# Kernel optimization log

Measured on AMD Instinct MI355X. Metric: run time of the kernel, lower is better.

## Reference

```python
import jax, jax.numpy as jnp
import numpy as np

NEG_INF = -1.0e15  # matches the module's self.infty


def setup_inputs() -> dict:
    key = jax.random.key(0)
    ks = jax.random.split(key, 12)
    B, N, D, H, HD = 256, 1024, 128, 8, 16
    inp = {
        "x": jax.random.normal(ks[0], (B, N, D), dtype=jnp.float32),
        "h_g": jax.random.normal(ks[1], (B, D), dtype=jnp.float32),
        "first": jax.random.normal(ks[2], (B, D), dtype=jnp.float32),
        "last": jax.random.normal(ks[3], (B, D), dtype=jnp.float32),
        "context": jax.random.normal(ks[4], (B, 2), dtype=jnp.float32),
        "K": jax.random.normal(ks[5], (B, H, N, HD), dtype=jnp.float32),
        "V": jax.random.normal(ks[6], (B, H, N, HD), dtype=jnp.float32),
        "K_lg": jax.random.normal(ks[7], (B, N, D), dtype=jnp.float32),
        "Wq": jax.random.normal(ks[8], (D, 3 * D + 2), dtype=jnp.float32) * 0.05,
        "bq": jnp.zeros((D,), dtype=jnp.float32),
        "Wo": jax.random.normal(ks[9], (D, D), dtype=jnp.float32) * 0.05,
        "bo": jnp.zeros((D,), dtype=jnp.float32),
        "mask": jax.random.randint(ks[10], (B, N), 0, 2, dtype=jnp.int32),
        "t": 1,
    }
    return inp


def reference(x, h_g, first, last, context, K, V, K_lg, Wq, bq, Wo, bo, mask, t):
    B, N, D = x.shape
    H, HD = K.shape[1], K.shape[3]
    # t > 0 path: context vector from graph embedding + first/last visited nodes
    h_c = jnp.concatenate([h_g, first, last, context], axis=1)  # [B, 3D+2]
    Q = h_c @ Wq.T + bq                                          # [B, D]
    Q = Q.reshape(B, H, HD)                                      # single query per head
    # masked single-query multi-head attention
    scale = jnp.sqrt(jnp.asarray(HD, dtype=x.dtype))
    scores = jnp.einsum("bhd,bhnd->bhn", Q, K) / scale          # [B, H, N]
    scores = jnp.where(mask[:, None, :] == 0, NEG_INF, scores)
    attn = jax.nn.softmax(scores, axis=-1)
    u = jnp.einsum("bhn,bhnd->bhd", attn, V).reshape(B, D)       # [B, D]
    u = u @ Wo.T + bo
    # pointer logits with tanh clipping
    logits = jnp.einsum("bd,bnd->bn", u, K_lg) / jnp.sqrt(jnp.asarray(D, dtype=x.dtype))
    logits = 10.0 * jnp.tanh(logits)
    logits = jnp.where(mask == 0, NEG_INF, logits)
    p = jax.nn.softmax(logits, axis=1)                           # [B, N]
    vertexes = jnp.argmax(p, axis=1)[:, None]                    # greedy (sample=False)
    probs = jnp.take_along_axis(p, vertexes, axis=1)             # [B, 1]
    return vertexes, probs
```

## Files before the change

### kernel.cpp

```cpp
#include <hip/hip_runtime.h>
#include <math.h>

#define Bn 256
#define Nn 1024
#define Dn 128
#define Hn 8
#define HDn 16
#define NEG_INF -1.0e15f

typedef float v4f __attribute__((ext_vector_type(4)));

__global__ __launch_bounds__(128) void k_q(
    const float* __restrict__ h_g, const float* __restrict__ first,
    const float* __restrict__ last, const float* __restrict__ context,
    const float* __restrict__ Wq, const float* __restrict__ bq,
    float* __restrict__ Qout)
{
    __shared__ __align__(16) float hc[3 * Dn + 2];
    const int b = blockIdx.x;
    const int t = threadIdx.x;
    hc[t]          = h_g[b * Dn + t];
    hc[Dn + t]     = first[b * Dn + t];
    hc[2 * Dn + t] = last[b * Dn + t];
    if (t < 2) hc[3 * Dn + t] = context[b * 2 + t];
    __syncthreads();

    const float2* w2 = (const float2*)(Wq + (size_t)t * (3 * Dn + 2));
    const float2* h2 = (const float2*)hc;
    float acc = bq[t];
#pragma unroll 8
    for (int k = 0; k < (3 * Dn + 2) / 2; ++k) {
        float2 w = w2[k], h = h2[k];
        acc = fmaf(w.x, h.x, fmaf(w.y, h.y, acc));
    }
    Qout[b * Dn + t] = acc;
}

__global__ __launch_bounds__(1024) void k_attn(
    const float* __restrict__ Q, const float* __restrict__ K,
    const float* __restrict__ V, const int* __restrict__ mask,
    float* __restrict__ Uout)
{
    __shared__ __align__(16) float sPart[16][Hn][20];
    __shared__ __align__(16) float sTot[Hn][20];

    const int b = blockIdx.x;
    const int tid = threadIdx.x;
    const int lane = tid & 63, wave = tid >> 6;
    const int g = tid & 3;
    const int kq = tid >> 2;

    const int* __restrict__ mrow = mask + (size_t)b * Nn;
    int mk[4];
#pragma unroll
    for (int p = 0; p < 4; ++p) mk[p] = mrow[p * 256 + kq];

    const float4* __restrict__ Qrow = (const float4*)(Q + (size_t)b * Dn);
    const float4* __restrict__ Kb = (const float4*)(K + (size_t)b * Hn * Nn * HDn);
    const float4* __restrict__ Vb = (const float4*)(V + (size_t)b * Hn * Nn * HDn);

#pragma unroll
    for (int s = 0; s < Hn; ++s) {
        const float4 qg = Qrow[s * 4 + g];
        const float4* __restrict__ Kh = Kb + (size_t)s * 4096;
        const float4* __restrict__ Vh = Vb + (size_t)s * 4096;

        float4 kf[4], vf[4];
#pragma unroll
        for (int p = 0; p < 4; ++p) kf[p] = Kh[p * 1024 + tid];
#pragma unroll
        for (int p = 0; p < 4; ++p) vf[p] = Vh[p * 1024 + tid];
        __builtin_amdgcn_sched_barrier(0);

        float4 u = {0.f, 0.f, 0.f, 0.f};
        float sum = 0.f;
#pragma unroll
        for (int p = 0; p < 4; ++p) {
            float sc = qg.x * kf[p].x + qg.y * kf[p].y + qg.z * kf[p].z + qg.w * kf[p].w;
            sc += __shfl_xor(sc, 1, 64);
            sc += __shfl_xor(sc, 2, 64);
            const float e = mk[p] ? __expf(sc * 0.25f) : 0.f;
            sum += e;
            u.x = fmaf(e, vf[p].x, u.x);
            u.y = fmaf(e, vf[p].y, u.y);
            u.z = fmaf(e, vf[p].z, u.z);
            u.w = fmaf(e, vf[p].w, u.w);
        }
#pragma unroll
        for (int o = 4; o <= 32; o <<= 1) {
            u.x += __shfl_xor(u.x, o, 64);
            u.y += __shfl_xor(u.y, o, 64);
            u.z += __shfl_xor(u.z, o, 64);
            u.w += __shfl_xor(u.w, o, 64);
            sum += __shfl_xor(sum, o, 64);
        }
        if (lane < 4) *(float4*)(&sPart[wave][s][lane * 4]) = u;
        if (lane == 0) sPart[wave][s][16] = sum;
    }
    __syncthreads();

    if (tid < Hn * 17) {
        const int s = tid / 17, j = tid % 17;
        float a = 0.f;
#pragma unroll
        for (int w = 0; w < 16; ++w) a += sPart[w][s][j];
        sTot[s][j] = a;
    }
    __syncthreads();
    if (tid < Dn) {
        const int s = tid >> 4, j = tid & 15;
        Uout[(size_t)b * Dn + tid] = sTot[s][j] / sTot[s][16];
    }
}

__global__ __launch_bounds__(1024) void k_ptr(
    const float* __restrict__ U, const float* __restrict__ Wo,
    const float* __restrict__ bo, const float* __restrict__ K_lg,
    const int* __restrict__ mask, float* __restrict__ out)
{
    __shared__ __align__(16) float sU[Dn];
    __shared__ __align__(16) float sU2[Dn];
    __shared__ __align__(16) float sL[Nn];
    __shared__ float sRv[16];
    __shared__ int   sRi[16];
    __shared__ float sRs[16];

    const int b = blockIdx.x;
    const int tid = threadIdx.x;
    const int lane = tid & 63, wave = tid >> 6;

    if (tid < Dn) sU[tid] = U[b * Dn + tid];
    __syncthreads();
    {
        const int d = tid >> 3, e8 = tid & 7;
        const float4* wrow = (const float4*)(Wo + (size_t)d * Dn + e8 * 16);
        const float4* su4 = (const float4*)(sU + e8 * 16);
        float acc = 0.f;
#pragma unroll
        for (int k = 0; k < 4; ++k) {
            const float4 w = wrow[k], u = su4[k];
            acc = fmaf(w.x, u.x, fmaf(w.y, u.y, fmaf(w.z, u.z, fmaf(w.w, u.w, acc))));
        }
        acc += __shfl_xor(acc, 1, 64);
        acc += __shfl_xor(acc, 2, 64);
        acc += __shfl_xor(acc, 4, 64);
        if (e8 == 0) sU2[d] = acc + bo[d];
    }
    __syncthreads();

    const v4f* __restrict__ Kl = (const v4f*)(K_lg + (size_t)b * Nn * Dn);
    const int* __restrict__ mrow = mask + (size_t)b * Nn;
    const int grp = tid >> 5, l32 = tid & 31;
    const v4f u2f = ((const v4f*)sU2)[l32];
    const float sc = 0.08838834764831845f;
#pragma unroll
    for (int it0 = 0; it0 < 32; it0 += 4) {
        v4f kl[4];
#pragma unroll
        for (int j = 0; j < 4; ++j)
            kl[j] = __builtin_nontemporal_load(&Kl[(size_t)(grp + 32 * (it0 + j)) * 32 + l32]);
        __builtin_amdgcn_sched_barrier(0);
#pragma unroll
        for (int j = 0; j < 4; ++j) {
            float p = kl[j].x * u2f.x + kl[j].y * u2f.y + kl[j].z * u2f.z + kl[j].w * u2f.w;
#pragma unroll
            for (int o = 16; o >= 1; o >>= 1) p += __shfl_xor(p, o, 64);
            if (l32 == 0) {
                const int n = grp + 32 * (it0 + j);
                sL[n] = (mrow[n] == 0) ? NEG_INF : 10.0f * tanhf(p * sc);
            }
        }
    }
    __syncthreads();

    float bv = sL[tid]; int bi = tid;
#pragma unroll
    for (int o = 32; o >= 1; o >>= 1) {
        const float ov = __shfl_xor(bv, o, 64);
        const int oi = __shfl_xor(bi, o, 64);
        if (ov > bv || (ov == bv && oi < bi)) { bv = ov; bi = oi; }
    }
    if (lane == 0) { sRv[wave] = bv; sRi[wave] = bi; }
    __syncthreads();
    bv = sRv[0]; bi = sRi[0];
#pragma unroll
    for (int w = 1; w < 16; ++w) {
        const float ov = sRv[w]; const int oi = sRi[w];
        if (ov > bv || (ov == bv && oi < bi)) { bv = ov; bi = oi; }
    }

    float lsum = __expf(sL[tid] - bv);
#pragma unroll
    for (int o = 32; o >= 1; o >>= 1) lsum += __shfl_xor(lsum, o, 64);
    if (lane == 0) sRs[wave] = lsum;
    __syncthreads();
    if (tid == 0) {
        float tot = 0.f;
#pragma unroll
        for (int w = 0; w < 16; ++w) tot += sRs[w];
        out[b] = (float)bi;
        out[Bn + b] = 1.0f / tot;
    }
}

extern "C" void kernel_launch(void* const* d_in, const int* in_sizes, int n_in,
                              void* d_out, int out_size, void* d_ws, size_t ws_size,
                              hipStream_t stream) {
    const float* h_g     = (const float*)d_in[1];
    const float* first   = (const float*)d_in[2];
    const float* last    = (const float*)d_in[3];
    const float* context = (const float*)d_in[4];
    const float* K       = (const float*)d_in[5];
    const float* V       = (const float*)d_in[6];
    const float* K_lg    = (const float*)d_in[7];
    const float* Wq      = (const float*)d_in[8];
    const float* bq      = (const float*)d_in[9];
    const float* Wo      = (const float*)d_in[10];
    const float* bo      = (const float*)d_in[11];
    const int*   mask    = (const int*)d_in[12];
    float* out = (float*)d_out;

    float* Qws = (float*)d_ws;
    float* Uws = Qws + Bn * Dn;

    k_q   <<<Bn,  128, 0, stream>>>(h_g, first, last, context, Wq, bq, Qws);
    k_attn<<<Bn, 1024, 0, stream>>>(Qws, K, V, mask, Uws);
    k_ptr <<<Bn, 1024, 0, stream>>>(Uws, Wo, bo, K_lg, mask, out);
}
```

Before: 106.6 us.

## Fuse query projection, attention and pointer kernels into one per-batch kernel

Merges the three kernels (Q projection, masked multi-head attention, pointer logits/argmax) into a single 1024-thread block per batch row, keeping Q and U in shared memory instead of round-tripping through the workspace. The Q projection is now split across 8 threads per output with shuffle reduction. Within the attention loop, V loads are issued after the scores are computed rather than together with K, and K_lg loads drop the nontemporal hint. This removes two launches and the intermediate global traffic, but the grid is only 256 blocks and the V loads now sit behind the score computation, which may expose more memory latency.

```diff
diff --git a/kernel.cpp b/kernel.cpp
--- a/kernel.cpp
+++ b/kernel.cpp
@@ -8,41 +8,25 @@
 #define HDn 16
 #define NEG_INF -1.0e15f
 
-typedef float v4f __attribute__((ext_vector_type(4)));
-
-__global__ __launch_bounds__(128) void k_q(
+__global__ __launch_bounds__(1024) void k_fused(
     const float* __restrict__ h_g, const float* __restrict__ first,
     const float* __restrict__ last, const float* __restrict__ context,
     const float* __restrict__ Wq, const float* __restrict__ bq,
-    float* __restrict__ Qout)
+    const float* __restrict__ K, const float* __restrict__ V,
+    const float* __restrict__ K_lg, const float* __restrict__ Wo,
+    const float* __restrict__ bo, const int* __restrict__ mask,
+    float* __restrict__ out)
 {
-    __shared__ __align__(16) float hc[3 * Dn + 2];
-    const int b = blockIdx.x;
-    const int t = threadIdx.x;
-    hc[t]          = h_g[b * Dn + t];
-    hc[Dn + t]     = first[b * Dn + t];
-    hc[2 * Dn + t] = last[b * Dn + t];
-    if (t < 2) hc[3 * Dn + t] = context[b * 2 + t];
-    __syncthreads();
-
-    const float2* w2 = (const float2*)(Wq + (size_t)t * (3 * Dn + 2));
-    const float2* h2 = (const float2*)hc;
-    float acc = bq[t];
-#pragma unroll 8
-    for (int k = 0; k < (3 * Dn + 2) / 2; ++k) {
-        float2 w = w2[k], h = h2[k];
-        acc = fmaf(w.x, h.x, fmaf(w.y, h.y, acc));
-    }
-    Qout[b * Dn + t] = acc;
-}
-
-__global__ __launch_bounds__(1024) void k_attn(
-    const float* __restrict__ Q, const float* __restrict__ K,
-    const float* __restrict__ V, const int* __restrict__ mask,
-    float* __restrict__ Uout)
-{
+    __shared__ __align__(16) float hc[392];
+    __shared__ __align__(16) float sQ[Dn];
     __shared__ __align__(16) float sPart[16][Hn][20];
     __shared__ __align__(16) float sTot[Hn][20];
+    __shared__ __align__(16) float sU[Dn];
+    __shared__ __align__(16) float sU2[Dn];
+    __shared__ __align__(16) float sL[Nn];
+    __shared__ float sRv[16];
+    __shared__ int   sRi[16];
+    __shared__ float sRs[16];
 
     const int b = blockIdx.x;
     const int tid = threadIdx.x;
@@ -50,41 +34,65 @@
     const int g = tid & 3;
     const int kq = tid >> 2;
 
+    if (tid < 128)      hc[tid] = h_g[b * 128 + tid];
+    else if (tid < 256) hc[tid] = first[b * 128 + tid - 128];
+    else if (tid < 384) hc[tid] = last[b * 128 + tid - 256];
+    else if (tid < 386) hc[tid] = context[b * 2 + tid - 384];
+    __syncthreads();
+
+    {
+        const int d = tid >> 3, e8 = tid & 7;
+        const int k0 = e8 * 48, k1 = (e8 == 7) ? 386 : (k0 + 48);
+        const float* __restrict__ wrow = Wq + (size_t)d * 386;
+        float acc = 0.f;
+        for (int k = k0; k < k1; ++k) acc = fmaf(wrow[k], hc[k], acc);
+        acc += __shfl_xor(acc, 1, 64);
+        acc += __shfl_xor(acc, 2, 64);
+        acc += __shfl_xor(acc, 4, 64);
+        if (e8 == 0) sQ[d] = acc + bq[d];
+    }
+
     const int* __restrict__ mrow = mask + (size_t)b * Nn;
     int mk[4];
 #pragma unroll
     for (int p = 0; p < 4; ++p) mk[p] = mrow[p * 256 + kq];
-
-    const float4* __restrict__ Qrow = (const float4*)(Q + (size_t)b * Dn);
+    __syncthreads();
+
     const float4* __restrict__ Kb = (const float4*)(K + (size_t)b * Hn * Nn * HDn);
     const float4* __restrict__ Vb = (const float4*)(V + (size_t)b * Hn * Nn * HDn);
 
 #pragma unroll
     for (int s = 0; s < Hn; ++s) {
-        const float4 qg = Qrow[s * 4 + g];
+        const float4 qg = ((const float4*)(sQ + s * HDn))[g];
         const float4* __restrict__ Kh = Kb + (size_t)s * 4096;
         const float4* __restrict__ Vh = Vb + (size_t)s * 4096;
 
-        float4 kf[4], vf[4];
+        float4 kf[4];
 #pragma unroll
         for (int p = 0; p < 4; ++p) kf[p] = Kh[p * 1024 + tid];
-#pragma unroll
-        for (int p = 0; p < 4; ++p) vf[p] = Vh[p * 1024 + tid];
-        __builtin_amdgcn_sched_barrier(0);
-
-        float4 u = {0.f, 0.f, 0.f, 0.f};
+        __builtin_amdgcn_sched_barrier(0);
+        float e[4];
         float sum = 0.f;
 #pragma unroll
         for (int p = 0; p < 4; ++p) {
             float sc = qg.x * kf[p].x + qg.y * kf[p].y + qg.z * kf[p].z + qg.w * kf[p].w;
             sc += __shfl_xor(sc, 1, 64);
             sc += __shfl_xor(sc, 2, 64);
-            const float e = mk[p] ? __expf(sc * 0.25f) : 0.f;
-            sum += e;
-            u.x = fmaf(e, vf[p].x, u.x);
-            u.y = fmaf(e, vf[p].y, u.y);
-            u.z = fmaf(e, vf[p].z, u.z);
-            u.w = fmaf(e, vf[p].w, u.w);
+            e[p] = mk[p] ? __expf(sc * 0.25f) : 0.f;
+            sum += e[p];
+        }
+        __builtin_amdgcn_sched_barrier(0);
+        float4 vf[4];
+#pragma unroll
+        for (int p = 0; p < 4; ++p) vf[p] = Vh[p * 1024 + tid];
+        __builtin_amdgcn_sched_barrier(0);
+        float4 u = {0.f, 0.f, 0.f, 0.f};
+#pragma unroll
+        for (int p = 0; p < 4; ++p) {
+            u.x = fmaf(e[p], vf[p].x, u.x);
+            u.y = fmaf(e[p], vf[p].y, u.y);
+            u.z = fmaf(e[p], vf[p].z, u.z);
+            u.w = fmaf(e[p], vf[p].w, u.w);
         }
 #pragma unroll
         for (int o = 4; o <= 32; o <<= 1) {
@@ -107,30 +115,9 @@
         sTot[s][j] = a;
     }
     __syncthreads();
-    if (tid < Dn) {
-        const int s = tid >> 4, j = tid & 15;
-        Uout[(size_t)b * Dn + tid] = sTot[s][j] / sTot[s][16];
-    }
-}
-
-__global__ __launch_bounds__(1024) void k_ptr(
-    const float* __restrict__ U, const float* __restrict__ Wo,
-    const float* __restrict__ bo, const float* __restrict__ K_lg,
-    const int* __restrict__ mask, float* __restrict__ out)
-{
-    __shared__ __align__(16) float sU[Dn];
-    __shared__ __align__(16) float sU2[Dn];
-    __shared__ __align__(16) float sL[Nn];
-    __shared__ float sRv[16];
-    __shared__ int   sRi[16];
-    __shared__ float sRs[16];
-
-    const int b = blockIdx.x;
-    const int tid = threadIdx.x;
-    const int lane = tid & 63, wave = tid >> 6;
-
-    if (tid < Dn) sU[tid] = U[b * Dn + tid];
-    __syncthreads();
+    if (tid < Dn) sU[tid] = sTot[tid >> 4][tid & 15] / sTot[tid >> 4][16];
+    __syncthreads();
+
     {
         const int d = tid >> 3, e8 = tid & 7;
         const float4* wrow = (const float4*)(Wo + (size_t)d * Dn + e8 * 16);
@@ -138,8 +125,8 @@
         float acc = 0.f;
 #pragma unroll
         for (int k = 0; k < 4; ++k) {
-            const float4 w = wrow[k], u = su4[k];
-            acc = fmaf(w.x, u.x, fmaf(w.y, u.y, fmaf(w.z, u.z, fmaf(w.w, u.w, acc))));
+            const float4 w = wrow[k], uu = su4[k];
+            acc = fmaf(w.x, uu.x, fmaf(w.y, uu.y, fmaf(w.z, uu.z, fmaf(w.w, uu.w, acc))));
         }
         acc += __shfl_xor(acc, 1, 64);
         acc += __shfl_xor(acc, 2, 64);
@@ -148,17 +135,16 @@
     }
     __syncthreads();
 
-    const v4f* __restrict__ Kl = (const v4f*)(K_lg + (size_t)b * Nn * Dn);
-    const int* __restrict__ mrow = mask + (size_t)b * Nn;
+    const float4* __restrict__ Kl = (const float4*)(K_lg + (size_t)b * Nn * Dn);
     const int grp = tid >> 5, l32 = tid & 31;
-    const v4f u2f = ((const v4f*)sU2)[l32];
+    const float4 u2f = ((const float4*)sU2)[l32];
     const float sc = 0.08838834764831845f;
 #pragma unroll
     for (int it0 = 0; it0 < 32; it0 += 4) {
-        v4f kl[4];
+        float4 kl[4];
 #pragma unroll
         for (int j = 0; j < 4; ++j)
-            kl[j] = __builtin_nontemporal_load(&Kl[(size_t)(grp + 32 * (it0 + j)) * 32 + l32]);
+            kl[j] = Kl[(size_t)(grp + 32 * (it0 + j)) * 32 + l32];
         __builtin_amdgcn_sched_barrier(0);
 #pragma unroll
         for (int j = 0; j < 4; ++j) {
@@ -220,10 +206,6 @@
     const int*   mask    = (const int*)d_in[12];
     float* out = (float*)d_out;
 
-    float* Qws = (float*)d_ws;
-    float* Uws = Qws + Bn * Dn;
-
-    k_q   <<<Bn,  128, 0, stream>>>(h_g, first, last, context, Wq, bq, Qws);
-    k_attn<<<Bn, 1024, 0, stream>>>(Qws, K, V, mask, Uws);
-    k_ptr <<<Bn, 1024, 0, stream>>>(Uws, Wo, bo, K_lg, mask, out);
+    k_fused<<<Bn, 1024, 0, stream>>>(h_g, first, last, context, Wq, bq,
+                                     K, V, K_lg, Wo, bo, mask, out);
 }
```

After: 134.4 us. +26.1%, slower.
